# Optimization experiments

Measured on AMD Instinct MI355X. Metric: run time of the kernel, lower is better.

The kernel has to match this reference:

```python
import jax, jax.numpy as jnp
import numpy as np

E = 100   # embedding_dim (Config)
H = 256   # hidden_dim (Config)


def setup_inputs() -> dict:
    key = jax.random.key(0)
    ks = jax.random.split(key, 16)
    V, T = 30000, 20
    B, L = 128, 512
    s = 0.05
    w = lambda k, shape: jax.random.normal(k, shape, dtype=jnp.float32) * s
    return {
        "sentences": jax.random.randint(ks[0], (B, L), 0, V, dtype=jnp.int32),
        "tags": jax.random.randint(ks[1], (B, L), 0, T, dtype=jnp.int32),
        "mask": jnp.ones((B, L), dtype=bool),
        "emb": w(ks[2], (V, E)),
        "Wih_f": w(ks[3], (4 * H, E)), "Whh_f": w(ks[4], (4 * H, H)),
        "bih_f": w(ks[5], (4 * H,)),   "bhh_f": w(ks[6], (4 * H,)),
        "Wih_b": w(ks[7], (4 * H, E)), "Whh_b": w(ks[8], (4 * H, H)),
        "bih_b": w(ks[9], (4 * H,)),   "bhh_b": w(ks[10], (4 * H,)),
        "Wout": w(ks[11], (T, 2 * H)), "bout": w(ks[12], (T,)),
        "trans": w(ks[13], (T, T)),
        "start_t": w(ks[14], (T,)),
        "end_t": w(ks[15], (T,)),
    }


def _lstm_dir(x, Wih, Whh, bih, bhh):
    # x: [B, L, E]; PyTorch gate order i, f, g, o; h0 = c0 = 0.
    B = x.shape[0]
    Hd = Whh.shape[1]
    b = bih + bhh

    def step(carry, xt):
        h, c = carry
        g = xt @ Wih.T + h @ Whh.T + b                      # [B, 4H]
        i, f, gg, o = jnp.split(g, 4, axis=-1)
        c = jax.nn.sigmoid(f) * c + jax.nn.sigmoid(i) * jnp.tanh(gg)
        h = jax.nn.sigmoid(o) * jnp.tanh(c)
        return (h, c), h

    init = (jnp.zeros((B, Hd), x.dtype), jnp.zeros((B, Hd), x.dtype))
    _, hs = jax.lax.scan(step, init, jnp.swapaxes(x, 0, 1))    # [L, B, H]
    return jnp.swapaxes(hs, 0, 1)


def _crf_nll(emissions, tags, mask, trans, start_t, end_t):
    # torchcrf log-likelihood with reduction='sum'; returns |-(llh)|.
    B, L, T = emissions.shape
    maskf = mask.astype(emissions.dtype)
    em_t = jnp.swapaxes(emissions, 0, 1)   # [L, B, T]
    tg_t = jnp.swapaxes(tags, 0, 1)        # [L, B]
    mk_t = jnp.swapaxes(maskf, 0, 1)       # [L, B]
    bidx = jnp.arange(B)

    # --- gold path score ---
    score0 = start_t[tags[:, 0]] + emissions[bidx, 0, tags[:, 0]]

    def score_step(s, inp):
        prev, cur, m, em = inp
        s = s + (trans[prev, cur] + em[bidx, cur]) * m
        return s, None

    score, _ = jax.lax.scan(score_step, score0,
                            (tg_t[:-1], tg_t[1:], mk_t[1:], em_t[1:]))
    seq_ends = mask.sum(axis=1).astype(jnp.int32) - 1
    last_tags = tags[bidx, seq_ends]
    score = score + end_t[last_tags]

    # --- log partition (forward algorithm) ---
    def alpha_step(a, inp):
        m, em = inp
        nxt = jax.nn.logsumexp(a[:, :, None] + trans[None] + em[:, None, :], axis=1)
        return jnp.where(m[:, None] > 0, nxt, a), None

    a0 = start_t[None, :] + em_t[0]
    alpha, _ = jax.lax.scan(alpha_step, a0, (mk_t[1:], em_t[1:]))
    logZ = jax.nn.logsumexp(alpha + end_t[None, :], axis=1)

    llh = jnp.sum(score - logZ)
    return jnp.abs(-llh)  # loss.mean() on a scalar is identity


def reference(sentences, tags, mask, emb, Wih_f, Whh_f, bih_f, bhh_f,
              Wih_b, Whh_b, bih_b, bhh_b, Wout, bout, trans, start_t, end_t):
    x = emb[sentences]                                           # [B, L, E]
    h_f = _lstm_dir(x, Wih_f, Whh_f, bih_f, bhh_f)               # [B, L, H]
    h_b = _lstm_dir(x[:, ::-1], Wih_b, Whh_b, bih_b, bhh_b)[:, ::-1]
    lstm_out = jnp.concatenate([h_f, h_b], axis=-1)              # [B, L, 2H]
    emissions = lstm_out @ Wout.T + bout                         # [B, L, T]
    return _crf_nll(emissions, tags, mask, trans, start_t, end_t)
```

## Files before the change

### kernel.cpp

```cpp
#include <hip/hip_runtime.h>


typedef float f32x4 __attribute__((ext_vector_type(4)));

#define MFMAF8(a, b, c) \
  __builtin_amdgcn_mfma_f32_16x16x32_fp8_fp8((a), (b), (c), 0, 0, 0)
#define ATOMIC_LD(p) __hip_atomic_load((p), __ATOMIC_RELAXED, __HIP_MEMORY_SCOPE_AGENT)
#define ATOMIC_ST(p, v) \
  __hip_atomic_store((p), (v), __ATOMIC_RELAXED, __HIP_MEMORY_SCOPE_AGENT)

__device__ __forceinline__ unsigned short f2bf(float x) {
  unsigned u = __float_as_uint(x);
  u += 0x7FFFu + ((u >> 16) & 1u);
  return (unsigned short)(u >> 16);
}
__device__ __forceinline__ float bf2f(unsigned short h) {
  return __uint_as_float(((unsigned)h) << 16);
}
__device__ __forceinline__ float sigm(float x) {
  return __builtin_amdgcn_rcpf(1.f + __expf(-x));
}
__device__ __forceinline__ float tanh_(float x) {
  float e = __expf(2.f * x);
  return (e - 1.f) * __builtin_amdgcn_rcpf(e + 1.f);
}
__device__ __forceinline__ unsigned pack_fp8x4(float a, float b, float c, float d) {
  int p = __builtin_amdgcn_cvt_pk_fp8_f32(a, b, 0, false);
  p = __builtin_amdgcn_cvt_pk_fp8_f32(c, d, p, true);
  return (unsigned)p;
}

__global__ __launch_bounds__(256) void prep_kernel(
    const float* __restrict__ Whh_f, const float* __restrict__ Whh_b,
    const float* __restrict__ Wih_f, const float* __restrict__ Wih_b,
    const float* __restrict__ Wout,
    const float* __restrict__ bih_f, const float* __restrict__ bhh_f,
    const float* __restrict__ bih_b, const float* __restrict__ bhh_b,
    long* __restrict__ whh, long* __restrict__ wih, long* __restrict__ wout,
    float* __restrict__ bias, int* __restrict__ flags) {
  int bid = blockIdx.x, tid = threadIdx.x;
  if (bid < 256) {
    int gid = bid * 256 + tid;
    int l = gid & 63, kt = (gid >> 6) & 7, n = (gid >> 9) & 63, dir = gid >> 15;
    const float* src = dir ? Whh_b : Whh_f;
    int row = n * 16 + (l & 15), k0 = kt * 32 + ((l >> 4) << 3);
    float v[8];
#pragma unroll
    for (int e = 0; e < 8; ++e) v[e] = src[row * 256 + k0 + e];
    unsigned lo = pack_fp8x4(v[0], v[1], v[2], v[3]);
    unsigned hi = pack_fp8x4(v[4], v[5], v[6], v[7]);
    whh[gid] = (long)lo | ((long)hi << 32);
  } else if (bid < 384) {
    int gid = (bid - 256) * 256 + tid;
    int l = gid & 63, kt = (gid >> 6) & 3, n = (gid >> 8) & 63, dir = gid >> 14;
    const float* src = dir ? Wih_b : Wih_f;
    int row = n * 16 + (l & 15), k0 = kt * 32 + ((l >> 4) << 3);
    float v[8];
#pragma unroll
    for (int e = 0; e < 8; ++e) {
      int k = k0 + e;
      v[e] = (k < 100) ? src[row * 100 + k] : 0.f;
    }
    unsigned lo = pack_fp8x4(v[0], v[1], v[2], v[3]);
    unsigned hi = pack_fp8x4(v[4], v[5], v[6], v[7]);
    wih[gid] = (long)lo | ((long)hi << 32);
  } else if (bid < 392) {
    int gid = (bid - 384) * 256 + tid;
    if (gid < 2048) {
      int l = gid & 63, kt = (gid >> 6) & 7, n = (gid >> 9) & 1, dir = gid >> 10;
      int colt = n * 16 + (l & 15), k0 = kt * 32 + ((l >> 4) << 3);
      float v[8];
#pragma unroll
      for (int e = 0; e < 8; ++e)
        v[e] = (colt < 20) ? Wout[colt * 512 + dir * 256 + k0 + e] : 0.f;
      unsigned lo = pack_fp8x4(v[0], v[1], v[2], v[3]);
      unsigned hi = pack_fp8x4(v[4], v[5], v[6], v[7]);
      wout[gid] = (long)lo | ((long)hi << 32);
    }
  } else if (bid < 400) {
    int idx = (bid - 392) * 256 + tid;
    if (idx < 2048) {
      int dir = idx >> 10, c = idx & 1023;
      bias[idx] = dir ? (bih_b[c] + bhh_b[c]) : (bih_f[c] + bhh_f[c]);
    }
  } else {
    if (tid < 64) flags[tid] = 0;
  }
}

__global__ __launch_bounds__(512) void lstm_kernel(
    const int* __restrict__ sent, const float* __restrict__ emb,
    const long* __restrict__ whh, const long* __restrict__ wih,
    const long* __restrict__ wout, const float* __restrict__ bias,
    float* __restrict__ em_out, unsigned char* __restrict__ h_glob,
    int* __restrict__ flags)
{
  __shared__ unsigned char h_lds[16][272];
  __shared__ unsigned char x_lds[2][16][136];
  __shared__ unsigned short g_T[256][18];
  __shared__ long wout_lds[2][8][64];
  __shared__ float bias_lds[1024];
  __shared__ long pad_lds[3456];

  const int tid = threadIdx.x;
  const int lid = tid & 63, w = tid >> 6;
  const int p = blockIdx.x & 15, q = blockIdx.x >> 4;
  const int dir = p >> 3, bt = p & 7, r0 = bt * 16;

  if (tid == 0) *(volatile long*)&pad_lds[0] = 0;

  const int arow = lid & 15;
  const int aq = lid >> 4;
  const int rb = aq * 4;
  const int g = w >> 1, s = w & 1;

  long wh[2][8], wx[2][4];
  {
    const long* whh_d = whh + dir * 32768;
    const long* wih_d = wih + dir * 16384;
#pragma unroll
    for (int n = 0; n < 2; ++n) {
      int nt = g * 16 + q * 4 + s * 2 + n;
#pragma unroll
      for (int j = 0; j < 8; ++j) {
        int kt = (2 * q + j) & 7;
        wh[n][j] = whh_d[(nt * 8 + kt) * 64 + lid];
      }
#pragma unroll
      for (int kt = 0; kt < 4; ++kt) wx[n][kt] = wih_d[(nt * 4 + kt) * 64 + lid];
    }
  }
#pragma unroll
  for (int n = 0; n < 2; ++n) {
#pragma unroll
    for (int j = 0; j < 8; ++j) asm volatile("" : "+v"(wh[n][j]));
#pragma unroll
    for (int kt = 0; kt < 4; ++kt) asm volatile("" : "+v"(wx[n][kt]));
  }

  {
    const long* wo_d = wout + dir * 1024;
    ((long*)wout_lds)[tid] = wo_d[tid];
    ((long*)wout_lds)[tid + 512] = wo_d[tid + 512];
    bias_lds[tid] = bias[dir * 1024 + tid];
    bias_lds[tid + 512] = bias[dir * 1024 + tid + 512];
  }
  for (int i = tid; i < 16 * 272; i += 512) ((unsigned char*)h_lds)[i] = 0;
  for (int i = tid; i < 2 * 16 * 136; i += 512) ((unsigned char*)x_lds)[i] = 0;

  const int ur = tid & 15, jb = (tid >> 4) * 2;
  float creg[2];
  creg[0] = 0.f;
  creg[1] = 0.f;

  unsigned* hb0 = (unsigned*)(h_glob + p * 4096);
  unsigned* hb1 = (unsigned*)(h_glob + 65536 + p * 4096);
  int* fl = flags + p * 4;

  const int pqa = (q + 1) & 3, pqb = (q + 2) & 3, pqc = (q + 3) & 3;

  const int rxA = tid / 25, cxA = tid - rxA * 25;
  const bool hasX = (tid < 400);

  if (hasX) {
    int t0 = dir ? 511 : 0;
    int sid = sent[(r0 + rxA) * 512 + t0];
    float4 v = *(const float4*)&emb[sid * 100 + cxA * 4];
    *(unsigned*)&x_lds[0][rxA][cxA * 4] = pack_fp8x4(v.x, v.y, v.z, v.w);
  }
  __syncthreads();

  const int prow = (tid & 255) >> 4, pwq = tid & 15;
  const bool roleA = (tid < 256);

  for (int t = 0; t < 512; ++t) {
    float4 xN;
    const bool haveN = hasX && (t < 511);
    if (haveN) {
      int te = dir ? (511 - (t + 1)) : (t + 1);
      int sid = sent[(r0 + rxA) * 512 + te];
      xN = *(const float4*)&emb[sid * 100 + cxA * 4];
    }

    unsigned wa = 0, wb2 = 0, wc = 0;
    if (t > 0) {
      if (tid < 3) {
        int pq = (q + 1 + tid) & 3;
        while (ATOMIC_LD(&fl[pq]) < t) __builtin_amdgcn_s_sleep(2);
      }
      __syncthreads();
      unsigned* srcw = (t & 1) ? hb0 : hb1;
      if (roleA) {
        wa = ATOMIC_LD(&srcw[prow * 64 + pqa * 16 + pwq]);
        wc = ATOMIC_LD(&srcw[prow * 64 + pqc * 16 + pwq]);
      } else {
        wb2 = ATOMIC_LD(&srcw[prow * 64 + pqb * 16 + pwq]);
      }
    }

    const unsigned char(*xb)[136] = (const unsigned char(*)[136])x_lds[t & 1];

    f32x4 acc[2];
#pragma unroll
    for (int n = 0; n < 2; ++n) {
      float bb = bias_lds[(g * 16 + q * 4 + s * 2 + n) * 16 + arow];
      f32x4 a = {bb, bb, bb, bb};
      acc[n] = a;
    }
#pragma unroll
    for (int j = 0; j < 2; ++j) {
      int kt = 2 * q + j;
      long a8 = *(const long*)&h_lds[arow][kt * 32 + aq * 8];
      acc[0] = MFMAF8(a8, wh[0][j], acc[0]);
      acc[1] = MFMAF8(a8, wh[1][j], acc[1]);
    }
#pragma unroll
    for (int kt = 0; kt < 4; ++kt) {
      long a8 = *(const long*)&xb[arow][kt * 32 + aq * 8];
      acc[0] = MFMAF8(a8, wx[0][kt], acc[0]);
      acc[1] = MFMAF8(a8, wx[1][kt], acc[1]);
    }

    if (t > 0) {
      if (roleA) {
        *(unsigned*)&h_lds[prow][pqa * 64 + pwq * 4] = wa;
        *(unsigned*)&h_lds[prow][pqc * 64 + pwq * 4] = wc;
      } else {
        *(unsigned*)&h_lds[prow][pqb * 64 + pwq * 4] = wb2;
      }
    }
    __syncthreads();

#pragma unroll
    for (int j = 2; j < 8; ++j) {
      int kt = (2 * q + j) & 7;
      long a8 = *(const long*)&h_lds[arow][kt * 32 + aq * 8];
      acc[0] = MFMAF8(a8, wh[0][j], acc[0]);
      acc[1] = MFMAF8(a8, wh[1][j], acc[1]);
    }
#pragma unroll
    for (int n = 0; n < 2; ++n) {
      int lcol = (w * 2 + n) * 16 + arow;
      *(unsigned*)&g_T[lcol][rb] =
          (unsigned)f2bf(acc[n][0]) | ((unsigned)f2bf(acc[n][1]) << 16);
      *(unsigned*)&g_T[lcol][rb + 2] =
          (unsigned)f2bf(acc[n][2]) | ((unsigned)f2bf(acc[n][3]) << 16);
    }

    if (t > 0 && w == 0 && (q == 1 || q == 2)) {
      int nt = q - 1;
      f32x4 e = {0.f, 0.f, 0.f, 0.f};
#pragma unroll
      for (int kt = 0; kt < 8; ++kt) {
        long a8 = *(const long*)&h_lds[arow][kt * 32 + aq * 8];
        e = MFMAF8(a8, wout_lds[nt][kt][lid], e);
      }
      int col = nt * 16 + arow;
      if (col < 20) {
        int tp = dir ? (512 - t) : (t - 1);
        int base = ((dir * 128 + r0 + rb) * 512 + tp) * 20 + col;
#pragma unroll
        for (int r = 0; r < 4; ++r) em_out[base + r * 10240] = e[r];
      }
    }
    __syncthreads();

    {
      float hv[2];
#pragma unroll
      for (int j = 0; j < 2; ++j) {
        int c = jb + j;
        float xi = bf2f(g_T[c][ur]);
        float xf = bf2f(g_T[64 + c][ur]);
        float xg = bf2f(g_T[128 + c][ur]);
        float xo = bf2f(g_T[192 + c][ur]);
        float cc = sigm(xf) * creg[j] + sigm(xi) * tanh_(xg);
        creg[j] = cc;
        hv[j] = sigm(xo) * tanh_(cc);
      }
      unsigned pk =
          (unsigned)__builtin_amdgcn_cvt_pk_fp8_f32(hv[0], hv[1], 0, false);
      *(unsigned short*)&h_lds[ur][q * 64 + jb] = (unsigned short)pk;
    }
    __syncthreads();

    {
      unsigned* dstw = (t & 1) ? hb1 : hb0;
      if (tid < 256) {
        int row = tid >> 4, wq = tid & 15;
        unsigned word = *(const unsigned*)&h_lds[row][q * 64 + wq * 4];
        ATOMIC_ST(&dstw[row * 64 + q * 16 + wq], word);
      }
    }
    if (haveN) {
      *(unsigned*)&x_lds[(t + 1) & 1][rxA][cxA * 4] =
          pack_fp8x4(xN.x, xN.y, xN.z, xN.w);
    }
    __syncthreads();
    if (tid == 0) ATOMIC_ST(&fl[q], t + 1);
  }

  if (tid < 3) {
    int pq = (q + 1 + tid) & 3;
    while (ATOMIC_LD(&fl[pq]) < 512) __builtin_amdgcn_s_sleep(2);
  }
  __syncthreads();
  {
    if (roleA) {
      unsigned wa2 = ATOMIC_LD(&hb1[prow * 64 + pqa * 16 + pwq]);
      unsigned wc2 = ATOMIC_LD(&hb1[prow * 64 + pqc * 16 + pwq]);
      *(unsigned*)&h_lds[prow][pqa * 64 + pwq * 4] = wa2;
      *(unsigned*)&h_lds[prow][pqc * 64 + pwq * 4] = wc2;
    } else {
      unsigned wb3 = ATOMIC_LD(&hb1[prow * 64 + pqb * 16 + pwq]);
      *(unsigned*)&h_lds[prow][pqb * 64 + pwq * 4] = wb3;
    }
  }
  __syncthreads();
  if (w == 0 && (q == 1 || q == 2)) {
    int nt = q - 1;
    f32x4 e = {0.f, 0.f, 0.f, 0.f};
#pragma unroll
    for (int kt = 0; kt < 8; ++kt) {
      long a8 = *(const long*)&h_lds[arow][kt * 32 + aq * 8];
      e = MFMAF8(a8, wout_lds[nt][kt][lid], e);
    }
    int col = nt * 16 + arow;
    if (col < 20) {
      int tp = dir ? 0 : 511;
      int base = ((dir * 128 + r0 + rb) * 512 + tp) * 20 + col;
#pragma unroll
      for (int r = 0; r < 4; ++r) em_out[base + r * 10240] = e[r];
    }
  }
}

__global__ __launch_bounds__(64) void crf_kernel(
    const float* __restrict__ emf, const float* __restrict__ embk,
    const int* __restrict__ tags, const int* __restrict__ maski,
    const float* __restrict__ bout, const float* __restrict__ trans,
    const float* __restrict__ start_t, const float* __restrict__ end_t,
    float* __restrict__ partial) {
  __shared__ float tr[400];
  const int b = blockIdx.x, tid = threadIdx.x;
  for (int i = tid; i < 400; i += 64) tr[i] = trans[i];
  __syncthreads();

  const int tp = tid;
  const bool act = tp < 20;
  float eT[20];
  if (act) {
#pragma unroll
    for (int t2 = 0; t2 < 20; ++t2) eT[t2] = __expf(tr[t2 * 20 + tp]);
  }
  const float* ef = emf + (size_t)b * 10240;
  const float* eb = embk + (size_t)b * 10240;
  const float bo = act ? bout[tp] : 0.f;

  float a = act ? (start_t[tp] + ef[tp] + eb[tp] + bo) : -1e30f;

  float efn = 0.f, ebn = 0.f;
  if (act) { efn = ef[20 + tp]; ebn = eb[20 + tp]; }

  for (int l = 1; l < 512; ++l) {
    float e_cur = efn + ebn + bo;
    if (act && l + 1 < 512) { efn = ef[(l + 1) * 20 + tp]; ebn = eb[(l + 1) * 20 + tp]; }
    float m = a;
#pragma unroll
    for (int o = 16; o > 0; o >>= 1) m = fmaxf(m, __shfl_xor(m, o, 32));
    float pv = __expf(a - m);
    float sgm = 0.f;
#pragma unroll
    for (int t2 = 0; t2 < 20; ++t2) sgm += __shfl(pv, t2, 32) * eT[t2];
    float anew = m + __logf(sgm) + e_cur;
    int mk = maski[b * 512 + l];
    if (act && mk) a = anew;
  }
  float v = act ? (a + end_t[tp]) : -1e30f;
  float m2 = v;
#pragma unroll
  for (int o = 16; o > 0; o >>= 1) m2 = fmaxf(m2, __shfl_xor(m2, o, 32));
  float s2 = __expf(v - m2);
#pragma unroll
  for (int o = 16; o > 0; o >>= 1) s2 += __shfl_xor(s2, o, 32);
  float logZ = m2 + __logf(s2);

  const int* tg = tags + b * 512;
  float sc = 0.f;
  int cnt = 0;
  for (int l = tid; l < 512; l += 64) {
    int mk = maski[b * 512 + l];
    cnt += mk ? 1 : 0;
    if (l >= 1 && mk) {
      int cur = tg[l], prev = tg[l - 1];
      sc += tr[prev * 20 + cur] + ef[l * 20 + cur] + eb[l * 20 + cur] + bout[cur];
    }
  }
#pragma unroll
  for (int o = 32; o > 0; o >>= 1) {
    sc += __shfl_xor(sc, o, 64);
    cnt += __shfl_xor(cnt, o, 64);
  }
  if (tid == 0) {
    int t0 = tg[0];
    sc += start_t[t0] + ef[t0] + eb[t0] + bout[t0];
    sc += end_t[tg[cnt - 1]];
    partial[b] = sc - logZ;
  }
}

__global__ __launch_bounds__(64) void final_kernel(const float* __restrict__ partial,
                                                   float* __restrict__ out) {
  int tid = threadIdx.x;
  float s = partial[tid] + partial[tid + 64];
#pragma unroll
  for (int o = 32; o > 0; o >>= 1) s += __shfl_xor(s, o, 64);
  if (tid == 0) out[0] = fabsf(s);
}

extern "C" void kernel_launch(void* const* d_in, const int* in_sizes, int n_in,
                              void* d_out, int out_size, void* d_ws, size_t ws_size,
                              hipStream_t stream) {
  const int* sent = (const int*)d_in[0];
  const int* tags = (const int*)d_in[1];
  const int* maski = (const int*)d_in[2];
  const float* emb = (const float*)d_in[3];
  const float* Wih_f = (const float*)d_in[4];
  const float* Whh_f = (const float*)d_in[5];
  const float* bih_f = (const float*)d_in[6];
  const float* bhh_f = (const float*)d_in[7];
  const float* Wih_b = (const float*)d_in[8];
  const float* Whh_b = (const float*)d_in[9];
  const float* bih_b = (const float*)d_in[10];
  const float* bhh_b = (const float*)d_in[11];
  const float* Wout = (const float*)d_in[12];
  const float* bout = (const float*)d_in[13];
  const float* trans = (const float*)d_in[14];
  const float* start_t = (const float*)d_in[15];
  const float* end_t = (const float*)d_in[16];

  char* ws = (char*)d_ws;
  float* em_base = (float*)ws;
  float* em_f = em_base;
  float* em_b = em_base + 128 * 512 * 20;
  long* whh_f8 = (long*)(ws + 10485760);
  long* wih_f8 = (long*)(ws + 11010048);
  long* wout_f8 = (long*)(ws + 11272192);
  float* bias_d = (float*)(ws + 11288576);
  float* partial = (float*)(ws + 11296768);
  int* flags = (int*)(ws + 11297280);
  unsigned char* h_glob = (unsigned char*)(ws + 11300864);

  prep_kernel<<<401, 256, 0, stream>>>(Whh_f, Whh_b, Wih_f, Wih_b, Wout,
                                       bih_f, bhh_f, bih_b, bhh_b,
                                       whh_f8, wih_f8, wout_f8, bias_d, flags);
  lstm_kernel<<<64, 512, 0, stream>>>(sent, emb, whh_f8, wih_f8, wout_f8,
                                      bias_d, em_base, h_glob, flags);
  crf_kernel<<<128, 64, 0, stream>>>(em_f, em_b, tags, maski, bout, trans,
                                     start_t, end_t, partial);
  final_kernel<<<1, 64, 0, stream>>>(partial, (float*)d_out);
}
```

Baseline: 1.332 ms.

## Replace per-step flag barrier with step-tagged 64-bit h units; move weights to LDS

```diff
diff --git a/kernel.cpp b/kernel.cpp
--- a/kernel.cpp
+++ b/kernel.cpp
@@ -2,11 +2,13 @@
 
 
 typedef float f32x4 __attribute__((ext_vector_type(4)));
+typedef unsigned long long u64;
 
 #define MFMAF8(a, b, c) \
   __builtin_amdgcn_mfma_f32_16x16x32_fp8_fp8((a), (b), (c), 0, 0, 0)
-#define ATOMIC_LD(p) __hip_atomic_load((p), __ATOMIC_RELAXED, __HIP_MEMORY_SCOPE_AGENT)
-#define ATOMIC_ST(p, v) \
+#define ATOMIC_LD64(p) \
+  __hip_atomic_load((p), __ATOMIC_RELAXED, __HIP_MEMORY_SCOPE_AGENT)
+#define ATOMIC_ST64(p, v) \
   __hip_atomic_store((p), (v), __ATOMIC_RELAXED, __HIP_MEMORY_SCOPE_AGENT)
 
 __device__ __forceinline__ unsigned short f2bf(float x) {
@@ -37,7 +39,7 @@
     const float* __restrict__ bih_f, const float* __restrict__ bhh_f,
     const float* __restrict__ bih_b, const float* __restrict__ bhh_b,
     long* __restrict__ whh, long* __restrict__ wih, long* __restrict__ wout,
-    float* __restrict__ bias, int* __restrict__ flags) {
+    float* __restrict__ bias, u64* __restrict__ units) {
   int bid = blockIdx.x, tid = threadIdx.x;
   if (bid < 256) {
     int gid = bid * 256 + tid;
@@ -84,7 +86,8 @@
       bias[idx] = dir ? (bih_b[c] + bhh_b[c]) : (bih_f[c] + bhh_f[c]);
     }
   } else {
-    if (tid < 64) flags[tid] = 0;
+    int base = (bid - 400) * 1024;
+    for (int i = tid; i < 1024; i += 256) units[base + i] = 0ull;
   }
 }
 
@@ -92,58 +95,48 @@
     const int* __restrict__ sent, const float* __restrict__ emb,
     const long* __restrict__ whh, const long* __restrict__ wih,
     const long* __restrict__ wout, const float* __restrict__ bias,
-    float* __restrict__ em_out, unsigned char* __restrict__ h_glob,
-    int* __restrict__ flags)
+    float* __restrict__ em_out, u64* __restrict__ units)
 {
+  __shared__ long whh_lds[16][8][64];
+  __shared__ long wih_lds[16][4][64];
   __shared__ unsigned char h_lds[16][272];
   __shared__ unsigned char x_lds[2][16][136];
   __shared__ unsigned short g_T[256][18];
   __shared__ long wout_lds[2][8][64];
-  __shared__ float bias_lds[1024];
-  __shared__ long pad_lds[3456];
+  __shared__ float bias_lds[256];
 
   const int tid = threadIdx.x;
   const int lid = tid & 63, w = tid >> 6;
   const int p = blockIdx.x & 15, q = blockIdx.x >> 4;
   const int dir = p >> 3, bt = p & 7, r0 = bt * 16;
 
-  if (tid == 0) *(volatile long*)&pad_lds[0] = 0;
-
   const int arow = lid & 15;
   const int aq = lid >> 4;
   const int rb = aq * 4;
   const int g = w >> 1, s = w & 1;
-
-  long wh[2][8], wx[2][4];
+  const int li0 = g * 4 + s * 2, li1 = li0 + 1;
+
   {
     const long* whh_d = whh + dir * 32768;
+    for (int idx = tid; idx < 8192; idx += 512) {
+      int li = idx >> 9, rem = idx & 511, kt = rem >> 6, ln = rem & 63;
+      int nt = (li >> 2) * 16 + q * 4 + (li & 3);
+      (&whh_lds[0][0][0])[idx] = whh_d[(nt * 8 + kt) * 64 + ln];
+    }
     const long* wih_d = wih + dir * 16384;
-#pragma unroll
-    for (int n = 0; n < 2; ++n) {
-      int nt = g * 16 + q * 4 + s * 2 + n;
-#pragma unroll
-      for (int j = 0; j < 8; ++j) {
-        int kt = (2 * q + j) & 7;
-        wh[n][j] = whh_d[(nt * 8 + kt) * 64 + lid];
-      }
-#pragma unroll
-      for (int kt = 0; kt < 4; ++kt) wx[n][kt] = wih_d[(nt * 4 + kt) * 64 + lid];
-    }
-  }
-#pragma unroll
-  for (int n = 0; n < 2; ++n) {
-#pragma unroll
-    for (int j = 0; j < 8; ++j) asm volatile("" : "+v"(wh[n][j]));
-#pragma unroll
-    for (int kt = 0; kt < 4; ++kt) asm volatile("" : "+v"(wx[n][kt]));
-  }
-
-  {
+    for (int idx = tid; idx < 4096; idx += 512) {
+      int li = idx >> 8, rem = idx & 255, kt = rem >> 6, ln = rem & 63;
+      int nt = (li >> 2) * 16 + q * 4 + (li & 3);
+      (&wih_lds[0][0][0])[idx] = wih_d[(nt * 4 + kt) * 64 + ln];
+    }
     const long* wo_d = wout + dir * 1024;
     ((long*)wout_lds)[tid] = wo_d[tid];
     ((long*)wout_lds)[tid + 512] = wo_d[tid + 512];
-    bias_lds[tid] = bias[dir * 1024 + tid];
-    bias_lds[tid + 512] = bias[dir * 1024 + tid + 512];
+    if (tid < 256) {
+      int li = tid >> 4, r = tid & 15;
+      int nt = (li >> 2) * 16 + q * 4 + (li & 3);
+      bias_lds[tid] = bias[dir * 1024 + nt * 16 + r];
+    }
   }
   for (int i = tid; i < 16 * 272; i += 512) ((unsigned char*)h_lds)[i] = 0;
   for (int i = tid; i < 2 * 16 * 136; i += 512) ((unsigned char*)x_lds)[i] = 0;
@@ -153,11 +146,11 @@
   creg[0] = 0.f;
   creg[1] = 0.f;
 
-  unsigned* hb0 = (unsigned*)(h_glob + p * 4096);
-  unsigned* hb1 = (unsigned*)(h_glob + 65536 + p * 4096);
-  int* fl = flags + p * 4;
+  u64* ub0 = units + (size_t)p * 1024;
+  u64* ub1 = units + (size_t)(16 + p) * 1024;
 
   const int pqa = (q + 1) & 3, pqb = (q + 2) & 3, pqc = (q + 3) & 3;
+  const int prow = (tid & 255) >> 4, pwi = tid & 15;
 
   const int rxA = tid / 25, cxA = tid - rxA * 25;
   const bool hasX = (tid < 400);
@@ -169,9 +162,6 @@
     *(unsigned*)&x_lds[0][rxA][cxA * 4] = pack_fp8x4(v.x, v.y, v.z, v.w);
   }
   __syncthreads();
-
-  const int prow = (tid & 255) >> 4, pwq = tid & 15;
-  const bool roleA = (tid < 256);
 
   for (int t = 0; t < 512; ++t) {
     float4 xN;
@@ -182,69 +172,71 @@
       xN = *(const float4*)&emb[sid * 100 + cxA * 4];
     }
 
-    unsigned wa = 0, wb2 = 0, wc = 0;
     if (t > 0) {
-      if (tid < 3) {
-        int pq = (q + 1 + tid) & 3;
-        while (ATOMIC_LD(&fl[pq]) < t) __builtin_amdgcn_s_sleep(2);
-      }
-      __syncthreads();
-      unsigned* srcw = (t & 1) ? hb0 : hb1;
-      if (roleA) {
-        wa = ATOMIC_LD(&srcw[prow * 64 + pqa * 16 + pwq]);
-        wc = ATOMIC_LD(&srcw[prow * 64 + pqc * 16 + pwq]);
+      u64* src = (t & 1) ? ub0 : ub1;
+      if (tid < 256) {
+        int ia = prow * 64 + pqa * 16 + pwi;
+        u64 va;
+        for (;;) {
+          va = ATOMIC_LD64(&src[ia]);
+          if ((unsigned)(va >> 32) == (unsigned)t) break;
+          __builtin_amdgcn_s_sleep(1);
+        }
+        *(unsigned*)&h_lds[prow][pqa * 64 + pwi * 4] = (unsigned)va;
       } else {
-        wb2 = ATOMIC_LD(&srcw[prow * 64 + pqb * 16 + pwq]);
-      }
-    }
+        int ia = prow * 64 + pqb * 16 + pwi;
+        int ib = prow * 64 + pqc * 16 + pwi;
+        u64 va = 0, vb = 0;
+        bool da = false, db = false;
+        for (;;) {
+          if (!da) {
+            va = ATOMIC_LD64(&src[ia]);
+            da = ((unsigned)(va >> 32) == (unsigned)t);
+          }
+          if (!db) {
+            vb = ATOMIC_LD64(&src[ib]);
+            db = ((unsigned)(vb >> 32) == (unsigned)t);
+          }
+          if (da && db) break;
+          __builtin_amdgcn_s_sleep(1);
+        }
+        *(unsigned*)&h_lds[prow][pqb * 64 + pwi * 4] = (unsigned)va;
+        *(unsigned*)&h_lds[prow][pqc * 64 + pwi * 4] = (unsigned)vb;
+      }
+    }
+    __syncthreads();
 
     const unsigned char(*xb)[136] = (const unsigned char(*)[136])x_lds[t & 1];
 
-    f32x4 acc[2];
-#pragma unroll
-    for (int n = 0; n < 2; ++n) {
-      float bb = bias_lds[(g * 16 + q * 4 + s * 2 + n) * 16 + arow];
-      f32x4 a = {bb, bb, bb, bb};
-      acc[n] = a;
-    }
-#pragma unroll
-    for (int j = 0; j < 2; ++j) {
-      int kt = 2 * q + j;
+    f32x4 acc0, acc1;
+    {
+      float b0 = bias_lds[li0 * 16 + arow], b1 = bias_lds[li1 * 16 + arow];
+      f32x4 a0 = {b0, b0, b0, b0}, a1 = {b1, b1, b1, b1};
+      acc0 = a0;
+      acc1 = a1;
+    }
+#pragma unroll
+    for (int kt = 0; kt < 8; ++kt) {
       long a8 = *(const long*)&h_lds[arow][kt * 32 + aq * 8];
-      acc[0] = MFMAF8(a8, wh[0][j], acc[0]);
-      acc[1] = MFMAF8(a8, wh[1][j], acc[1]);
+      acc0 = MFMAF8(a8, whh_lds[li0][kt][lid], acc0);
+      acc1 = MFMAF8(a8, whh_lds[li1][kt][lid], acc1);
     }
 #pragma unroll
     for (int kt = 0; kt < 4; ++kt) {
       long a8 = *(const long*)&xb[arow][kt * 32 + aq * 8];
-      acc[0] = MFMAF8(a8, wx[0][kt], acc[0]);
-      acc[1] = MFMAF8(a8, wx[1][kt], acc[1]);
-    }
-
-    if (t > 0) {
-      if (roleA) {
-        *(unsigned*)&h_lds[prow][pqa * 64 + pwq * 4] = wa;
-        *(unsigned*)&h_lds[prow][pqc * 64 + pwq * 4] = wc;
-      } else {
-        *(unsigned*)&h_lds[prow][pqb * 64 + pwq * 4] = wb2;
-      }
-    }
-    __syncthreads();
-
-#pragma unroll
-    for (int j = 2; j < 8; ++j) {
-      int kt = (2 * q + j) & 7;
-      long a8 = *(const long*)&h_lds[arow][kt * 32 + aq * 8];
-      acc[0] = MFMAF8(a8, wh[0][j], acc[0]);
-      acc[1] = MFMAF8(a8, wh[1][j], acc[1]);
-    }
-#pragma unroll
-    for (int n = 0; n < 2; ++n) {
-      int lcol = (w * 2 + n) * 16 + arow;
-      *(unsigned*)&g_T[lcol][rb] =
-          (unsigned)f2bf(acc[n][0]) | ((unsigned)f2bf(acc[n][1]) << 16);
-      *(unsigned*)&g_T[lcol][rb + 2] =
-          (unsigned)f2bf(acc[n][2]) | ((unsigned)f2bf(acc[n][3]) << 16);
+      acc0 = MFMAF8(a8, wih_lds[li0][kt][lid], acc0);
+      acc1 = MFMAF8(a8, wih_lds[li1][kt][lid], acc1);
+    }
+    {
+      int lcol0 = li0 * 16 + arow, lcol1 = li1 * 16 + arow;
+      *(unsigned*)&g_T[lcol0][rb] =
+          (unsigned)f2bf(acc0[0]) | ((unsigned)f2bf(acc0[1]) << 16);
+      *(unsigned*)&g_T[lcol0][rb + 2] =
+          (unsigned)f2bf(acc0[2]) | ((unsigned)f2bf(acc0[3]) << 16);
+      *(unsigned*)&g_T[lcol1][rb] =
+          (unsigned)f2bf(acc1[0]) | ((unsigned)f2bf(acc1[1]) << 16);
+      *(unsigned*)&g_T[lcol1][rb + 2] =
+          (unsigned)f2bf(acc1[2]) | ((unsigned)f2bf(acc1[3]) << 16);
     }
 
     if (t > 0 && w == 0 && (q == 1 || q == 2)) {
@@ -282,55 +274,66 @@
           (unsigned)__builtin_amdgcn_cvt_pk_fp8_f32(hv[0], hv[1], 0, false);
       *(unsigned short*)&h_lds[ur][q * 64 + jb] = (unsigned short)pk;
     }
-    __syncthreads();
-
-    {
-      unsigned* dstw = (t & 1) ? hb1 : hb0;
-      if (tid < 256) {
-        int row = tid >> 4, wq = tid & 15;
-        unsigned word = *(const unsigned*)&h_lds[row][q * 64 + wq * 4];
-        ATOMIC_ST(&dstw[row * 64 + q * 16 + wq], word);
-      }
-    }
     if (haveN) {
       *(unsigned*)&x_lds[(t + 1) & 1][rxA][cxA * 4] =
           pack_fp8x4(xN.x, xN.y, xN.z, xN.w);
     }
     __syncthreads();
-    if (tid == 0) ATOMIC_ST(&fl[q], t + 1);
-  }
-
-  if (tid < 3) {
-    int pq = (q + 1 + tid) & 3;
-    while (ATOMIC_LD(&fl[pq]) < 512) __builtin_amdgcn_s_sleep(2);
-  }
-  __syncthreads();
-  {
-    if (roleA) {
-      unsigned wa2 = ATOMIC_LD(&hb1[prow * 64 + pqa * 16 + pwq]);
-      unsigned wc2 = ATOMIC_LD(&hb1[prow * 64 + pqc * 16 + pwq]);
-      *(unsigned*)&h_lds[prow][pqa * 64 + pwq * 4] = wa2;
-      *(unsigned*)&h_lds[prow][pqc * 64 + pwq * 4] = wc2;
+
+    if (tid < 256) {
+      unsigned data = *(const unsigned*)&h_lds[prow][q * 64 + pwi * 4];
+      u64 unit = ((u64)(unsigned)(t + 1) << 32) | (u64)data;
+      u64* dst = (t & 1) ? ub1 : ub0;
+      ATOMIC_ST64(&dst[prow * 64 + q * 16 + pwi], unit);
+    }
+  }
+
+  if (q == 1 || q == 2) {
+    if (tid < 256) {
+      int ia = prow * 64 + pqa * 16 + pwi;
+      u64 va;
+      for (;;) {
+        va = ATOMIC_LD64(&ub1[ia]);
+        if ((unsigned)(va >> 32) == 512u) break;
+        __builtin_amdgcn_s_sleep(1);
+      }
+      *(unsigned*)&h_lds[prow][pqa * 64 + pwi * 4] = (unsigned)va;
     } else {
-      unsigned wb3 = ATOMIC_LD(&hb1[prow * 64 + pqb * 16 + pwq]);
-      *(unsigned*)&h_lds[prow][pqb * 64 + pwq * 4] = wb3;
-    }
-  }
-  __syncthreads();
-  if (w == 0 && (q == 1 || q == 2)) {
-    int nt = q - 1;
-    f32x4 e = {0.f, 0.f, 0.f, 0.f};
-#pragma unroll
-    for (int kt = 0; kt < 8; ++kt) {
-      long a8 = *(const long*)&h_lds[arow][kt * 32 + aq * 8];
-      e = MFMAF8(a8, wout_lds[nt][kt][lid], e);
-    }
-    int col = nt * 16 + arow;
-    if (col < 20) {
-      int tp = dir ? 0 : 511;
-      int base = ((dir * 128 + r0 + rb) * 512 + tp) * 20 + col;
-#pragma unroll
-      for (int r = 0; r < 4; ++r) em_out[base + r * 10240] = e[r];
+      int ia = prow * 64 + pqb * 16 + pwi;
+      int ib = prow * 64 + pqc * 16 + pwi;
+      u64 va = 0, vb = 0;
+      bool da = false, db = false;
+      for (;;) {
+        if (!da) {
+          va = ATOMIC_LD64(&ub1[ia]);
+          da = ((unsigned)(va >> 32) == 512u);
+        }
+        if (!db) {
+          vb = ATOMIC_LD64(&ub1[ib]);
+          db = ((unsigned)(vb >> 32) == 512u);
+        }
+        if (da && db) break;
+        __builtin_amdgcn_s_sleep(1);
+      }
+      *(unsigned*)&h_lds[prow][pqb * 64 + pwi * 4] = (unsigned)va;
+      *(unsigned*)&h_lds[prow][pqc * 64 + pwi * 4] = (unsigned)vb;
+    }
+    __syncthreads();
+    if (w == 0) {
+      int nt = q - 1;
+      f32x4 e = {0.f, 0.f, 0.f, 0.f};
+#pragma unroll
+      for (int kt = 0; kt < 8; ++kt) {
+        long a8 = *(const long*)&h_lds[arow][kt * 32 + aq * 8];
+        e = MFMAF8(a8, wout_lds[nt][kt][lid], e);
+      }
+      int col = nt * 16 + arow;
+      if (col < 20) {
+        int tp = dir ? 0 : 511;
+        int base = ((dir * 128 + r0 + rb) * 512 + tp) * 20 + col;
+#pragma unroll
+        for (int r = 0; r < 4; ++r) em_out[base + r * 10240] = e[r];
+      }
     }
   }
 }
@@ -448,14 +451,13 @@
   long* wout_f8 = (long*)(ws + 11272192);
   float* bias_d = (float*)(ws + 11288576);
   float* partial = (float*)(ws + 11296768);
-  int* flags = (int*)(ws + 11297280);
-  unsigned char* h_glob = (unsigned char*)(ws + 11300864);
-
-  prep_kernel<<<401, 256, 0, stream>>>(Whh_f, Whh_b, Wih_f, Wih_b, Wout,
+  u64* units = (u64*)(ws + 11297280);
+
+  prep_kernel<<<432, 256, 0, stream>>>(Whh_f, Whh_b, Wih_f, Wih_b, Wout,
                                        bih_f, bhh_f, bih_b, bhh_b,
-                                       whh_f8, wih_f8, wout_f8, bias_d, flags);
+                                       whh_f8, wih_f8, wout_f8, bias_d, units);
   lstm_kernel<<<64, 512, 0, stream>>>(sent, emb, whh_f8, wih_f8, wout_f8,
-                                      bias_d, em_base, h_glob, flags);
+                                      bias_d, em_base, units);
   crf_kernel<<<128, 64, 0, stream>>>(em_f, em_b, tags, maski, bout, trans,
                                      start_t, end_t, partial);
   final_kernel<<<1, 64, 0, stream>>>(partial, (float*)d_out);
```

Result: slower. 1.422 ms (+6.7%).

## Move LSTM weights to LDS and publish h directly to global without extra barrier

Applied to the files above, without the earlier changes.

```diff
diff --git a/kernel.cpp b/kernel.cpp
--- a/kernel.cpp
+++ b/kernel.cpp
@@ -95,55 +95,46 @@
     float* __restrict__ em_out, unsigned char* __restrict__ h_glob,
     int* __restrict__ flags)
 {
+  __shared__ long whh_lds[16][8][64];
+  __shared__ long wih_lds[16][4][64];
   __shared__ unsigned char h_lds[16][272];
   __shared__ unsigned char x_lds[2][16][136];
   __shared__ unsigned short g_T[256][18];
   __shared__ long wout_lds[2][8][64];
-  __shared__ float bias_lds[1024];
-  __shared__ long pad_lds[3456];
+  __shared__ float bias_lds[256];
 
   const int tid = threadIdx.x;
   const int lid = tid & 63, w = tid >> 6;
   const int p = blockIdx.x & 15, q = blockIdx.x >> 4;
   const int dir = p >> 3, bt = p & 7, r0 = bt * 16;
 
-  if (tid == 0) *(volatile long*)&pad_lds[0] = 0;
-
   const int arow = lid & 15;
   const int aq = lid >> 4;
   const int rb = aq * 4;
   const int g = w >> 1, s = w & 1;
-
-  long wh[2][8], wx[2][4];
+  const int li0 = g * 4 + s * 2, li1 = li0 + 1;
+
   {
     const long* whh_d = whh + dir * 32768;
+    for (int idx = tid; idx < 8192; idx += 512) {
+      int li = idx >> 9, rem = idx & 511, kt = rem >> 6, ln = rem & 63;
+      int nt = (li >> 2) * 16 + q * 4 + (li & 3);
+      (&whh_lds[0][0][0])[idx] = whh_d[(nt * 8 + kt) * 64 + ln];
+    }
     const long* wih_d = wih + dir * 16384;
-#pragma unroll
-    for (int n = 0; n < 2; ++n) {
-      int nt = g * 16 + q * 4 + s * 2 + n;
-#pragma unroll
-      for (int j = 0; j < 8; ++j) {
-        int kt = (2 * q + j) & 7;
-        wh[n][j] = whh_d[(nt * 8 + kt) * 64 + lid];
-      }
-#pragma unroll
-      for (int kt = 0; kt < 4; ++kt) wx[n][kt] = wih_d[(nt * 4 + kt) * 64 + lid];
-    }
-  }
-#pragma unroll
-  for (int n = 0; n < 2; ++n) {
-#pragma unroll
-    for (int j = 0; j < 8; ++j) asm volatile("" : "+v"(wh[n][j]));
-#pragma unroll
-    for (int kt = 0; kt < 4; ++kt) asm volatile("" : "+v"(wx[n][kt]));
-  }
-
-  {
+    for (int idx = tid; idx < 4096; idx += 512) {
+      int li = idx >> 8, rem = idx & 255, kt = rem >> 6, ln = rem & 63;
+      int nt = (li >> 2) * 16 + q * 4 + (li & 3);
+      (&wih_lds[0][0][0])[idx] = wih_d[(nt * 4 + kt) * 64 + ln];
+    }
     const long* wo_d = wout + dir * 1024;
     ((long*)wout_lds)[tid] = wo_d[tid];
     ((long*)wout_lds)[tid + 512] = wo_d[tid + 512];
-    bias_lds[tid] = bias[dir * 1024 + tid];
-    bias_lds[tid + 512] = bias[dir * 1024 + tid + 512];
+    if (tid < 256) {
+      int li = tid >> 4, r = tid & 15;
+      int nt = (li >> 2) * 16 + q * 4 + (li & 3);
+      bias_lds[tid] = bias[dir * 1024 + nt * 16 + r];
+    }
   }
   for (int i = tid; i < 16 * 272; i += 512) ((unsigned char*)h_lds)[i] = 0;
   for (int i = tid; i < 2 * 16 * 136; i += 512) ((unsigned char*)x_lds)[i] = 0;
@@ -158,6 +149,8 @@
   int* fl = flags + p * 4;
 
   const int pqa = (q + 1) & 3, pqb = (q + 2) & 3, pqc = (q + 3) & 3;
+  const int prow = (tid & 255) >> 4, pwi = tid & 15;
+  const bool roleA = (tid < 256);
 
   const int rxA = tid / 25, cxA = tid - rxA * 25;
   const bool hasX = (tid < 400);
@@ -169,9 +162,6 @@
     *(unsigned*)&x_lds[0][rxA][cxA * 4] = pack_fp8x4(v.x, v.y, v.z, v.w);
   }
   __syncthreads();
-
-  const int prow = (tid & 255) >> 4, pwq = tid & 15;
-  const bool roleA = (tid < 256);
 
   for (int t = 0; t < 512; ++t) {
     float4 xN;
@@ -191,42 +181,42 @@
       __syncthreads();
       unsigned* srcw = (t & 1) ? hb0 : hb1;
       if (roleA) {
-        wa = ATOMIC_LD(&srcw[prow * 64 + pqa * 16 + pwq]);
-        wc = ATOMIC_LD(&srcw[prow * 64 + pqc * 16 + pwq]);
+        wa = ATOMIC_LD(&srcw[prow * 64 + pqa * 16 + pwi]);
+        wc = ATOMIC_LD(&srcw[prow * 64 + pqc * 16 + pwi]);
       } else {
-        wb2 = ATOMIC_LD(&srcw[prow * 64 + pqb * 16 + pwq]);
+        wb2 = ATOMIC_LD(&srcw[prow * 64 + pqb * 16 + pwi]);
       }
     }
 
     const unsigned char(*xb)[136] = (const unsigned char(*)[136])x_lds[t & 1];
 
-    f32x4 acc[2];
-#pragma unroll
-    for (int n = 0; n < 2; ++n) {
-      float bb = bias_lds[(g * 16 + q * 4 + s * 2 + n) * 16 + arow];
-      f32x4 a = {bb, bb, bb, bb};
-      acc[n] = a;
+    f32x4 acc0, acc1;
+    {
+      float b0 = bias_lds[li0 * 16 + arow], b1 = bias_lds[li1 * 16 + arow];
+      f32x4 a0 = {b0, b0, b0, b0}, a1 = {b1, b1, b1, b1};
+      acc0 = a0;
+      acc1 = a1;
     }
 #pragma unroll
     for (int j = 0; j < 2; ++j) {
       int kt = 2 * q + j;
       long a8 = *(const long*)&h_lds[arow][kt * 32 + aq * 8];
-      acc[0] = MFMAF8(a8, wh[0][j], acc[0]);
-      acc[1] = MFMAF8(a8, wh[1][j], acc[1]);
+      acc0 = MFMAF8(a8, whh_lds[li0][kt][lid], acc0);
+      acc1 = MFMAF8(a8, whh_lds[li1][kt][lid], acc1);
     }
 #pragma unroll
     for (int kt = 0; kt < 4; ++kt) {
       long a8 = *(const long*)&xb[arow][kt * 32 + aq * 8];
-      acc[0] = MFMAF8(a8, wx[0][kt], acc[0]);
-      acc[1] = MFMAF8(a8, wx[1][kt], acc[1]);
+      acc0 = MFMAF8(a8, wih_lds[li0][kt][lid], acc0);
+      acc1 = MFMAF8(a8, wih_lds[li1][kt][lid], acc1);
     }
 
     if (t > 0) {
       if (roleA) {
-        *(unsigned*)&h_lds[prow][pqa * 64 + pwq * 4] = wa;
-        *(unsigned*)&h_lds[prow][pqc * 64 + pwq * 4] = wc;
+        *(unsigned*)&h_lds[prow][pqa * 64 + pwi * 4] = wa;
+        *(unsigned*)&h_lds[prow][pqc * 64 + pwi * 4] = wc;
       } else {
-        *(unsigned*)&h_lds[prow][pqb * 64 + pwq * 4] = wb2;
+        *(unsigned*)&h_lds[prow][pqb * 64 + pwi * 4] = wb2;
       }
     }
     __syncthreads();
@@ -235,16 +225,19 @@
     for (int j = 2; j < 8; ++j) {
       int kt = (2 * q + j) & 7;
       long a8 = *(const long*)&h_lds[arow][kt * 32 + aq * 8];
-      acc[0] = MFMAF8(a8, wh[0][j], acc[0]);
-      acc[1] = MFMAF8(a8, wh[1][j], acc[1]);
-    }
-#pragma unroll
-    for (int n = 0; n < 2; ++n) {
-      int lcol = (w * 2 + n) * 16 + arow;
-      *(unsigned*)&g_T[lcol][rb] =
-          (unsigned)f2bf(acc[n][0]) | ((unsigned)f2bf(acc[n][1]) << 16);
-      *(unsigned*)&g_T[lcol][rb + 2] =
-          (unsigned)f2bf(acc[n][2]) | ((unsigned)f2bf(acc[n][3]) << 16);
+      acc0 = MFMAF8(a8, whh_lds[li0][kt][lid], acc0);
+      acc1 = MFMAF8(a8, whh_lds[li1][kt][lid], acc1);
+    }
+    {
+      int lcol0 = li0 * 16 + arow, lcol1 = li1 * 16 + arow;
+      *(unsigned*)&g_T[lcol0][rb] =
+          (unsigned)f2bf(acc0[0]) | ((unsigned)f2bf(acc0[1]) << 16);
+      *(unsigned*)&g_T[lcol0][rb + 2] =
+          (unsigned)f2bf(acc0[2]) | ((unsigned)f2bf(acc0[3]) << 16);
+      *(unsigned*)&g_T[lcol1][rb] =
+          (unsigned)f2bf(acc1[0]) | ((unsigned)f2bf(acc1[1]) << 16);
+      *(unsigned*)&g_T[lcol1][rb + 2] =
+          (unsigned)f2bf(acc1[2]) | ((unsigned)f2bf(acc1[3]) << 16);
     }
 
     if (t > 0 && w == 0 && (q == 1 || q == 2)) {
@@ -281,16 +274,9 @@
       unsigned pk =
           (unsigned)__builtin_amdgcn_cvt_pk_fp8_f32(hv[0], hv[1], 0, false);
       *(unsigned short*)&h_lds[ur][q * 64 + jb] = (unsigned short)pk;
-    }
-    __syncthreads();
-
-    {
-      unsigned* dstw = (t & 1) ? hb1 : hb0;
-      if (tid < 256) {
-        int row = tid >> 4, wq = tid & 15;
-        unsigned word = *(const unsigned*)&h_lds[row][q * 64 + wq * 4];
-        ATOMIC_ST(&dstw[row * 64 + q * 16 + wq], word);
-      }
+      unsigned short* dst16 =
+          (unsigned short*)((t & 1) ? hb1 : hb0);
+      ATOMIC_ST(&dst16[ur * 128 + ((q * 64 + jb) >> 1)], (unsigned short)pk);
     }
     if (haveN) {
       *(unsigned*)&x_lds[(t + 1) & 1][rxA][cxA * 4] =
@@ -300,37 +286,37 @@
     if (tid == 0) ATOMIC_ST(&fl[q], t + 1);
   }
 
-  if (tid < 3) {
-    int pq = (q + 1 + tid) & 3;
-    while (ATOMIC_LD(&fl[pq]) < 512) __builtin_amdgcn_s_sleep(2);
-  }
-  __syncthreads();
-  {
+  if (q == 1 || q == 2) {
+    if (tid < 3) {
+      int pq = (q + 1 + tid) & 3;
+      while (ATOMIC_LD(&fl[pq]) < 512) __builtin_amdgcn_s_sleep(2);
+    }
+    __syncthreads();
     if (roleA) {
-      unsigned wa2 = ATOMIC_LD(&hb1[prow * 64 + pqa * 16 + pwq]);
-      unsigned wc2 = ATOMIC_LD(&hb1[prow * 64 + pqc * 16 + pwq]);
-      *(unsigned*)&h_lds[prow][pqa * 64 + pwq * 4] = wa2;
-      *(unsigned*)&h_lds[prow][pqc * 64 + pwq * 4] = wc2;
+      unsigned wa2 = ATOMIC_LD(&hb1[prow * 64 + pqa * 16 + pwi]);
+      unsigned wc2 = ATOMIC_LD(&hb1[prow * 64 + pqc * 16 + pwi]);
+      *(unsigned*)&h_lds[prow][pqa * 64 + pwi * 4] = wa2;
+      *(unsigned*)&h_lds[prow][pqc * 64 + pwi * 4] = wc2;
     } else {
-      unsigned wb3 = ATOMIC_LD(&hb1[prow * 64 + pqb * 16 + pwq]);
-      *(unsigned*)&h_lds[prow][pqb * 64 + pwq * 4] = wb3;
-    }
-  }
-  __syncthreads();
-  if (w == 0 && (q == 1 || q == 2)) {
-    int nt = q - 1;
-    f32x4 e = {0.f, 0.f, 0.f, 0.f};
-#pragma unroll
-    for (int kt = 0; kt < 8; ++kt) {
-      long a8 = *(const long*)&h_lds[arow][kt * 32 + aq * 8];
-      e = MFMAF8(a8, wout_lds[nt][kt][lid], e);
-    }
-    int col = nt * 16 + arow;
-    if (col < 20) {
-      int tp = dir ? 0 : 511;
-      int base = ((dir * 128 + r0 + rb) * 512 + tp) * 20 + col;
-#pragma unroll
-      for (int r = 0; r < 4; ++r) em_out[base + r * 10240] = e[r];
+      unsigned wb3 = ATOMIC_LD(&hb1[prow * 64 + pqb * 16 + pwi]);
+      *(unsigned*)&h_lds[prow][pqb * 64 + pwi * 4] = wb3;
+    }
+    __syncthreads();
+    if (w == 0) {
+      int nt = q - 1;
+      f32x4 e = {0.f, 0.f, 0.f, 0.f};
+#pragma unroll
+      for (int kt = 0; kt < 8; ++kt) {
+        long a8 = *(const long*)&h_lds[arow][kt * 32 + aq * 8];
+        e = MFMAF8(a8, wout_lds[nt][kt][lid], e);
+      }
+      int col = nt * 16 + arow;
+      if (col < 20) {
+        int tp = dir ? 0 : 511;
+        int base = ((dir * 128 + r0 + rb) * 512 + tp) * 20 + col;
+#pragma unroll
+        for (int r = 0; r < 4; ++r) em_out[base + r * 10240] = e[r];
+      }
     }
   }
 }
```

Result: slower. 1.360 ms (+2.1%).
